# Kernel tuning notes

Hardware: AMD Instinct MI355X
Metric: run time of the kernel (lower is better)

The kernel has to match this reference:

```python
import jax, jax.numpy as jnp
import numpy as np


def reference(key, value, time_decay, time_first):
    # key, value: [B, T, H]; time_decay/time_first: [H]
    u = time_first
    w = -jnp.exp(time_decay)
    B, T, H = key.shape

    def step(carry, kv):
        a, b, exponent = carry  # each [B, H]
        kt, vt = kv             # [B, H] each
        # numerically stabilized WKV output at this timestep
        max_e = jnp.maximum(exponent, u + kt)
        wt = jnp.exp(u + kt - max_e)
        scale = jnp.exp(exponent - max_e)
        wkv = (a * scale + wt * vt) / (b * scale + wt)
        # state update with decay w
        max_e2 = jnp.maximum(exponent + w, kt)
        s1 = jnp.exp(exponent + w - max_e2)
        s2 = jnp.exp(kt - max_e2)
        a_new = s1 * a + s2 * vt
        b_new = s1 * b + s2
        return (a_new, b_new, max_e2), wkv

    init = (
        jnp.zeros((B, H), dtype=key.dtype),
        jnp.zeros((B, H), dtype=key.dtype),
        jnp.full((B, H), -jnp.inf, dtype=key.dtype),
    )
    k_t = jnp.transpose(key, (1, 0, 2))    # [T, B, H]
    v_t = jnp.transpose(value, (1, 0, 2))  # [T, B, H]
    _, out = jax.lax.scan(step, init, (k_t, v_t))
    return jnp.transpose(out, (1, 0, 2))   # [B, T, H]


def setup_inputs() -> dict:
    k = jax.random.key(0)
    k1, k2, k3, k4 = jax.random.split(k, 4)
    B, T, H = 8, 2048, 768
    return {
        "key": jax.random.normal(k1, (B, T, H), dtype=jnp.float32),
        "value": jax.random.normal(k2, (B, T, H), dtype=jnp.float32),
        "time_decay": jax.random.normal(k3, (H,), dtype=jnp.float32),
        "time_first": jax.random.normal(k4, (H,), dtype=jnp.float32),
    }
```

## Files before the change

kernel.cpp:

```cpp
#include <hip/hip_runtime.h>
#include <math.h>


#define B_   8
#define T_   2048
#define H_   768
#define H4_  (H_/4)
#define NC_  64
#define L_   32
#define HO4_ 8
#define NT_  512
#define PAD_ 33
#define SCAN_STEPS 6

__global__ __launch_bounds__(NT_) void wkv_fused(
    const float* __restrict__ key, const float* __restrict__ val,
    const float* __restrict__ time_decay, const float* __restrict__ time_first,
    float* __restrict__ out)
{
    __shared__ float sa[NC_][PAD_];
    __shared__ float sb[NC_][PAD_];
    __shared__ float se[NC_][PAD_];

    const int tid = threadIdx.x;
    const int ho4 = tid & (HO4_ - 1);
    const int c   = tid >> 3;
    const int h0  = blockIdx.x * (HO4_ * 4) + ho4 * 4;
    const int b   = blockIdx.y;
    const int col = ho4 * 4;

    const float4 td4 = *(const float4*)(time_decay + h0);
    const float4 tf4 = *(const float4*)(time_first + h0);
    float w[4], u[4];
    w[0] = -__expf(td4.x); w[1] = -__expf(td4.y);
    w[2] = -__expf(td4.z); w[3] = -__expf(td4.w);
    u[0] = tf4.x; u[1] = tf4.y; u[2] = tf4.z; u[3] = tf4.w;

    const size_t base = ((size_t)b * T_ + (size_t)c * L_) * H_ + h0;
    const float4* kp = (const float4*)(key + base);
    const float4* vp = (const float4*)(val + base);

    float a[4]  = {0.f, 0.f, 0.f, 0.f};
    float bb[4] = {0.f, 0.f, 0.f, 0.f};
    float e[4]  = {-INFINITY, -INFINITY, -INFINITY, -INFINITY};

#pragma unroll 4
    for (int t = 0; t < L_; ++t) {
        const float4 k4 = kp[(size_t)t * H4_];
        const float4 v4 = vp[(size_t)t * H4_];
        const float kt[4] = {k4.x, k4.y, k4.z, k4.w};
        const float vt[4] = {v4.x, v4.y, v4.z, v4.w};
#pragma unroll
        for (int j = 0; j < 4; ++j) {
            const float ew = e[j] + w[j];
            const float m2 = fmaxf(ew, kt[j]);
            const float s1 = __expf(ew - m2);
            const float s2 = __expf(kt[j] - m2);
            a[j]  = fmaf(s1, a[j],  s2 * vt[j]);
            bb[j] = fmaf(s1, bb[j], s2);
            e[j]  = m2;
        }
    }

#pragma unroll
    for (int j = 0; j < 4; ++j) {
        sa[c][col + j] = a[j];
        sb[c][col + j] = bb[j];
        se[c][col + j] = e[j];
    }
    __syncthreads();

#pragma unroll
    for (int s = 0; s < SCAN_STEPS; ++s) {
        const int d = 1 << s;
        const bool act = (c >= d);
        float pa[4], pb[4], pe[4];
        if (act) {
#pragma unroll
            for (int j = 0; j < 4; ++j) {
                pa[j] = sa[c - d][col + j];
                pb[j] = sb[c - d][col + j];
                pe[j] = se[c - d][col + j] + w[j] * (float)(L_ * d);
            }
        }
        __syncthreads();
        if (act) {
#pragma unroll
            for (int j = 0; j < 4; ++j) {
                const float m = fmaxf(pe[j], e[j]);
                const float x = __expf(pe[j] - m);
                const float y = __expf(e[j] - m);
                a[j]  = fmaf(pa[j], x, a[j] * y);
                bb[j] = fmaf(pb[j], x, bb[j] * y);
                e[j]  = m;
                sa[c][col + j] = a[j];
                sb[c][col + j] = bb[j];
                se[c][col + j] = e[j];
            }
        }
        __syncthreads();
    }

    float ra[4] = {0.f, 0.f, 0.f, 0.f};
    float rb[4] = {0.f, 0.f, 0.f, 0.f};
    float re[4] = {-INFINITY, -INFINITY, -INFINITY, -INFINITY};
    if (c > 0) {
#pragma unroll
        for (int j = 0; j < 4; ++j) {
            ra[j] = sa[c - 1][col + j];
            rb[j] = sb[c - 1][col + j];
            re[j] = se[c - 1][col + j];
        }
    }

    float4* op = (float4*)(out + base);
#pragma unroll 4
    for (int t = 0; t < L_; ++t) {
        const float4 k4 = kp[(size_t)t * H4_];
        const float4 v4 = vp[(size_t)t * H4_];
        const float kt[4] = {k4.x, k4.y, k4.z, k4.w};
        const float vt[4] = {v4.x, v4.y, v4.z, v4.w};
        float o[4];
#pragma unroll
        for (int j = 0; j < 4; ++j) {
            const float uk = u[j] + kt[j];
            const float m1 = fmaxf(re[j], uk);
            const float wt = __expf(uk - m1);
            const float sc = __expf(re[j] - m1);
            const float num = fmaf(ra[j], sc, wt * vt[j]);
            const float den = fmaf(rb[j], sc, wt);
            o[j] = __fdividef(num, den);

            const float ew = re[j] + w[j];
            const float m2 = fmaxf(ew, kt[j]);
            const float s1 = __expf(ew - m2);
            const float s2 = __expf(kt[j] - m2);
            ra[j] = fmaf(s1, ra[j], s2 * vt[j]);
            rb[j] = fmaf(s1, rb[j], s2);
            re[j] = m2;
        }
        float4 o4;
        o4.x = o[0]; o4.y = o[1]; o4.z = o[2]; o4.w = o[3];
        op[(size_t)t * H4_] = o4;
    }
}

extern "C" void kernel_launch(void* const* d_in, const int* in_sizes, int n_in,
                              void* d_out, int out_size, void* d_ws, size_t ws_size,
                              hipStream_t stream) {
    const float* key = (const float*)d_in[0];
    const float* val = (const float*)d_in[1];
    const float* td  = (const float*)d_in[2];
    const float* tf  = (const float*)d_in[3];
    float* out = (float*)d_out;

    dim3 grid(H_ / (HO4_ * 4), B_);
    wkv_fused<<<grid, NT_, 0, stream>>>(key, val, td, tf, out);
}
```

Measured before the change: 178.5 us.

## Split WKV scan into two kernels with quarter-level carry propagation

The single fused kernel becomes two launches. The first computes per-chunk states over shorter chunks (16 steps instead of 32) in four time quarters per sequence, then writes exclusive prefixes and quarter totals to workspace. The second combines the totals of earlier quarters, applies them to each chunk's prefix, and replays the chunk to produce outputs. This gives four times more blocks at half the block size, for better occupancy and shorter serial loops, at the cost of a second launch and workspace traffic.

Result: faster. 163.5 us (-8.4%).

```diff
diff --git a/kernel.cpp b/kernel.cpp
--- a/kernel.cpp
+++ b/kernel.cpp
@@ -2,41 +2,48 @@
 #include <math.h>
 
 
-#define B_   8
-#define T_   2048
-#define H_   768
-#define H4_  (H_/4)
-#define NC_  64
-#define L_   32
-#define HO4_ 8
-#define NT_  512
-#define PAD_ 33
-#define SCAN_STEPS 6
-
-__global__ __launch_bounds__(NT_) void wkv_fused(
+#define B_    8
+#define T_    2048
+#define H_    768
+#define H4_   (H_/4)
+#define NQ_   4
+#define NCB_  32
+#define L_    16
+#define QLEN_ (NCB_*L_)
+#define HS_   (H_/32)
+#define HO4_  8
+#define NT_   256
+#define PAD_  33
+
+#define EXCL_N ((size_t)B_*HS_*NQ_*NCB_*32)
+#define TOT_N  ((size_t)B_*HS_*NQ_*32)
+
+__global__ __launch_bounds__(NT_) void wkv_p1(
     const float* __restrict__ key, const float* __restrict__ val,
-    const float* __restrict__ time_decay, const float* __restrict__ time_first,
-    float* __restrict__ out)
+    const float* __restrict__ time_decay,
+    float* __restrict__ ea, float* __restrict__ eb, float* __restrict__ ee,
+    float* __restrict__ ta, float* __restrict__ tb, float* __restrict__ te)
 {
-    __shared__ float sa[NC_][PAD_];
-    __shared__ float sb[NC_][PAD_];
-    __shared__ float se[NC_][PAD_];
+    __shared__ float sa[NCB_][PAD_];
+    __shared__ float sb[NCB_][PAD_];
+    __shared__ float se[NCB_][PAD_];
 
     const int tid = threadIdx.x;
     const int ho4 = tid & (HO4_ - 1);
     const int c   = tid >> 3;
-    const int h0  = blockIdx.x * (HO4_ * 4) + ho4 * 4;
-    const int b   = blockIdx.y;
     const int col = ho4 * 4;
+    const int hs  = blockIdx.x;
+    const int q   = blockIdx.y;
+    const int b   = blockIdx.z;
+    const int h0  = hs * 32 + col;
 
     const float4 td4 = *(const float4*)(time_decay + h0);
-    const float4 tf4 = *(const float4*)(time_first + h0);
-    float w[4], u[4];
+    float w[4];
     w[0] = -__expf(td4.x); w[1] = -__expf(td4.y);
     w[2] = -__expf(td4.z); w[3] = -__expf(td4.w);
-    u[0] = tf4.x; u[1] = tf4.y; u[2] = tf4.z; u[3] = tf4.w;
-
-    const size_t base = ((size_t)b * T_ + (size_t)c * L_) * H_ + h0;
+
+    const int cg = q * NCB_ + c;
+    const size_t base = ((size_t)b * T_ + (size_t)cg * L_) * H_ + h0;
     const float4* kp = (const float4*)(key + base);
     const float4* vp = (const float4*)(val + base);
 
@@ -71,7 +78,7 @@
     __syncthreads();
 
 #pragma unroll
-    for (int s = 0; s < SCAN_STEPS; ++s) {
+    for (int s = 0; s < 5; ++s) {
         const int d = 1 << s;
         const bool act = (c >= d);
         float pa[4], pb[4], pe[4];
@@ -101,19 +108,109 @@
         __syncthreads();
     }
 
-    float ra[4] = {0.f, 0.f, 0.f, 0.f};
-    float rb[4] = {0.f, 0.f, 0.f, 0.f};
-    float re[4] = {-INFINITY, -INFINITY, -INFINITY, -INFINITY};
+    float xa[4] = {0.f, 0.f, 0.f, 0.f};
+    float xb[4] = {0.f, 0.f, 0.f, 0.f};
+    float xe[4] = {-INFINITY, -INFINITY, -INFINITY, -INFINITY};
     if (c > 0) {
 #pragma unroll
         for (int j = 0; j < 4; ++j) {
-            ra[j] = sa[c - 1][col + j];
-            rb[j] = sb[c - 1][col + j];
-            re[j] = se[c - 1][col + j];
-        }
-    }
-
-    float4* op = (float4*)(out + base);
+            xa[j] = sa[c - 1][col + j];
+            xb[j] = sb[c - 1][col + j];
+            xe[j] = se[c - 1][col + j];
+        }
+    }
+
+    const size_t eoff = ((((size_t)b * HS_ + hs) * NQ_ + q) * NCB_ + c) * 32 + col;
+#pragma unroll
+    for (int j = 0; j < 4; ++j) {
+        ea[eoff + j] = xa[j];
+        eb[eoff + j] = xb[j];
+        ee[eoff + j] = xe[j];
+    }
+    if (c == NCB_ - 1) {
+        const size_t toff = (((size_t)b * HS_ + hs) * NQ_ + q) * 32 + col;
+#pragma unroll
+        for (int j = 0; j < 4; ++j) {
+            ta[toff + j] = a[j];
+            tb[toff + j] = bb[j];
+            te[toff + j] = e[j];
+        }
+    }
+}
+
+__global__ __launch_bounds__(NT_) void wkv_p2(
+    const float* __restrict__ key, const float* __restrict__ val,
+    const float* __restrict__ time_decay, const float* __restrict__ time_first,
+    const float* __restrict__ ea, const float* __restrict__ eb,
+    const float* __restrict__ ee,
+    const float* __restrict__ ta, const float* __restrict__ tb,
+    const float* __restrict__ te,
+    float* __restrict__ out)
+{
+    const int tid = threadIdx.x;
+    const int ho4 = tid & (HO4_ - 1);
+    const int c   = tid >> 3;
+    const int col = ho4 * 4;
+    const int hs  = blockIdx.x;
+    const int q   = blockIdx.y;
+    const int b   = blockIdx.z;
+    const int h0  = hs * 32 + col;
+
+    const float4 td4 = *(const float4*)(time_decay + h0);
+    const float4 tf4 = *(const float4*)(time_first + h0);
+    float w[4], u[4];
+    w[0] = -__expf(td4.x); w[1] = -__expf(td4.y);
+    w[2] = -__expf(td4.z); w[3] = -__expf(td4.w);
+    u[0] = tf4.x; u[1] = tf4.y; u[2] = tf4.z; u[3] = tf4.w;
+
+    const size_t eoff = ((((size_t)b * HS_ + hs) * NQ_ + q) * NCB_ + c) * 32 + col;
+    float ra[4], rb[4], re[4];
+#pragma unroll
+    for (int j = 0; j < 4; ++j) {
+        ra[j] = ea[eoff + j];
+        rb[j] = eb[eoff + j];
+        re[j] = ee[eoff + j];
+    }
+
+    float pa[4] = {0.f, 0.f, 0.f, 0.f};
+    float pb[4] = {0.f, 0.f, 0.f, 0.f};
+    float pe[4] = {-INFINITY, -INFINITY, -INFINITY, -INFINITY};
+    for (int qq = 0; qq < q; ++qq) {
+        const size_t toff = (((size_t)b * HS_ + hs) * NQ_ + qq) * 32 + col;
+#pragma unroll
+        for (int j = 0; j < 4; ++j) {
+            const float Ta = ta[toff + j];
+            const float Tb = tb[toff + j];
+            const float Te = te[toff + j];
+            const float sh = pe[j] + w[j] * (float)QLEN_;
+            const float m  = fmaxf(sh, Te);
+            const float x  = __expf(sh - m);
+            const float y  = __expf(Te - m);
+            pa[j] = fmaf(pa[j], x, Ta * y);
+            pb[j] = fmaf(pb[j], x, Tb * y);
+            pe[j] = m;
+        }
+    }
+
+#pragma unroll
+    for (int j = 0; j < 4; ++j) {
+        const float sh = pe[j] + w[j] * (float)(c * L_);
+        const float m  = fmaxf(sh, re[j]);
+        if (m > -INFINITY) {
+            const float x = __expf(sh - m);
+            const float y = __expf(re[j] - m);
+            ra[j] = fmaf(pa[j], x, ra[j] * y);
+            rb[j] = fmaf(pb[j], x, rb[j] * y);
+            re[j] = m;
+        }
+    }
+
+    const int cg = q * NCB_ + c;
+    const size_t base = ((size_t)b * T_ + (size_t)cg * L_) * H_ + h0;
+    const float4* kp = (const float4*)(key + base);
+    const float4* vp = (const float4*)(val + base);
+    float4*       op = (float4*)(out + base);
+
 #pragma unroll 4
     for (int t = 0; t < L_; ++t) {
         const float4 k4 = kp[(size_t)t * H4_];
@@ -154,6 +251,14 @@
     const float* tf  = (const float*)d_in[3];
     float* out = (float*)d_out;
 
-    dim3 grid(H_ / (HO4_ * 4), B_);
-    wkv_fused<<<grid, NT_, 0, stream>>>(key, val, td, tf, out);
+    float* ea = (float*)d_ws;
+    float* eb = ea + EXCL_N;
+    float* ee = eb + EXCL_N;
+    float* ta = ee + EXCL_N;
+    float* tb = ta + TOT_N;
+    float* te = tb + TOT_N;
+
+    dim3 grid(HS_, NQ_, B_);
+    wkv_p1<<<grid, NT_, 0, stream>>>(key, val, td, ea, eb, ee, ta, tb, te);
+    wkv_p2<<<grid, NT_, 0, stream>>>(key, val, td, tf, ea, eb, ee, ta, tb, te, out);
 }
```
